# Optimization experiments

Hardware: AMD Instinct MI355X
Metric: run time of the kernel (lower is better)

The kernel has to match this reference:

```python
import jax, jax.numpy as jnp
import numpy as np

N_NODES = 100000
N_EDGES = 3200000
IN_DIM = 128
H1, F1 = 8, 8          # layer1: 8 heads x 8 feats -> concat 64
N_CLASSES = 40         # layer2: 1 head -> classes
NEG_SLOPE = 0.2        # GAT LeakyReLU slope


def setup_inputs() -> dict:
    key = jax.random.key(0)
    ks = jax.random.split(key, 8)
    x = jax.random.normal(ks[0], (N_NODES, IN_DIM), dtype=jnp.float32)
    adj = jax.random.randint(ks[1], (2, N_EDGES), 0, N_NODES, dtype=jnp.int64)
    s1 = 1.0 / np.sqrt(IN_DIM)
    s2 = 1.0 / np.sqrt(H1 * F1)
    W1 = jax.random.normal(ks[2], (IN_DIM, H1 * F1), dtype=jnp.float32) * s1
    a1_src = jax.random.normal(ks[3], (H1, F1), dtype=jnp.float32) * s2
    a1_dst = jax.random.normal(ks[4], (H1, F1), dtype=jnp.float32) * s2
    W2 = jax.random.normal(ks[5], (H1 * F1, N_CLASSES), dtype=jnp.float32) * s2
    a2_src = jax.random.normal(ks[6], (1, N_CLASSES), dtype=jnp.float32) * s2
    a2_dst = jax.random.normal(ks[7], (1, N_CLASSES), dtype=jnp.float32) * s2
    return {"input_matrix": x, "adjacency_coo_matrix": adj,
            "W1": W1, "a1_src": a1_src, "a1_dst": a1_dst,
            "W2": W2, "a2_src": a2_src, "a2_dst": a2_dst}


def gat_layer(x, src, dst, W, a_s, a_d, heads, fdim):
    n = x.shape[0]
    h = (x @ W).reshape(n, heads, fdim)                 # [N,H,F]
    e_src = jnp.sum(h * a_s, axis=-1)                   # [N,H]
    e_dst = jnp.sum(h * a_d, axis=-1)                   # [N,H]
    e = jax.nn.leaky_relu(e_src[src] + e_dst[dst], NEG_SLOPE)  # [E,H]
    m = jax.ops.segment_max(e, dst, num_segments=n)     # per-dst softmax max
    p = jnp.exp(e - m[dst])
    s = jax.ops.segment_sum(p, dst, num_segments=n)
    alpha = p / s[dst]                                  # [E,H]
    out = jax.ops.segment_sum(alpha[:, :, None] * h[src], dst, num_segments=n)
    return out                                          # [N,H,F]


def reference(input_matrix, adjacency_coo_matrix, W1, a1_src, a1_dst, W2, a2_src, a2_dst):
    n = input_matrix.shape[0]
    loops = jnp.arange(n, dtype=adjacency_coo_matrix.dtype)
    src = jnp.concatenate([adjacency_coo_matrix[0], loops])
    dst = jnp.concatenate([adjacency_coo_matrix[1], loops])
    x = gat_layer(input_matrix, src, dst, W1, a1_src, a1_dst, H1, F1)
    x = jax.nn.elu(x.reshape(n, H1 * F1))               # concat heads + ELU
    x = gat_layer(x, src, dst, W2, a2_src, a2_dst, 1, N_CLASSES)
    return jax.nn.log_softmax(x.reshape(n, N_CLASSES), axis=1)
```

## Files before the change

kernel.cpp:

```cpp
#include <hip/hip_runtime.h>
#include <hip/hip_fp16.h>
#include <math.h>

#define NN 100000
#define EE 3200000
#define ET (EE + NN)
#define BKW 128
#define NBK ((NN + BKW - 1) / BKW)
#define BCAP 5120
#define EPB 4096
#define NB_P1 ((EE + EPB - 1) / EPB)
#define NB_G 391

typedef float v2f __attribute__((ext_vector_type(2)));
typedef float v4f __attribute__((ext_vector_type(4)));
typedef _Float16 v8h __attribute__((ext_vector_type(8)));

__device__ __forceinline__ float lrelu(float v) { return fmaxf(v, 0.2f * v); }

__device__ __forceinline__ unsigned char to_fp8(float v) {
  return (unsigned char)(__builtin_amdgcn_cvt_pk_fp8_f32(v, v, 0, false) & 0xff);
}


__global__ __launch_bounds__(256) void k_p1(const int* __restrict__ srcs,
                                            const int* __restrict__ dsts,
                                            int* __restrict__ bcount,
                                            int* __restrict__ bbuf) {
  __shared__ int lcnt[NBK];
  __shared__ int lbase[NBK];
  int tid = threadIdx.x;
  for (int i = tid; i < NBK; i += 256) lcnt[i] = 0;
  __syncthreads();
  int e0 = blockIdx.x * EPB;
  int rank[16], bkt[16], pk[16];
#pragma unroll
  for (int i = 0; i < 16; ++i) {
    int e = e0 + tid + i * 256;
    bkt[i] = -1;
    if (e < EE) {
      int d = dsts[e];
      int s = srcs[e];
      int b = d >> 7;
      rank[i] = atomicAdd(&lcnt[b], 1);
      bkt[i] = b;
      pk[i] = (s << 7) | (d & 127);
    }
  }
  __syncthreads();
  for (int i = tid; i < NBK; i += 256) {
    int c = lcnt[i];
    lbase[i] = c ? atomicAdd(&bcount[i], c) : 0;
  }
  __syncthreads();
#pragma unroll
  for (int i = 0; i < 16; ++i) {
    if (bkt[i] >= 0) {
      bbuf[(size_t)bkt[i] * BCAP + lbase[bkt[i]] + rank[i]] = pk[i];
    }
  }
}

__global__ void k_bscan(const int* __restrict__ bcount, int* __restrict__ bbase) {
  __shared__ int s[1024];
  int t = threadIdx.x;
  int v = 0;
  if (t < NBK) v = bcount[t] + min(BKW, NN - (t << 7));
  s[t] = v;
  __syncthreads();
  for (int off = 1; off < 1024; off <<= 1) {
    int u = (t >= off) ? s[t - off] : 0;
    __syncthreads();
    s[t] += u;
    __syncthreads();
  }
  if (t < NBK) bbase[t] = s[t] - v;
}

__global__ __launch_bounds__(256) void k_p2(const int* __restrict__ bcount,
                                            const int* __restrict__ bbase,
                                            const int* __restrict__ bbuf,
                                            int* __restrict__ offsets,
                                            int* __restrict__ edge_src) {
  __shared__ int cnt[BKW];
  __shared__ int s1[BKW];
  __shared__ int cur[BKW];
  int b = blockIdx.x, tid = threadIdx.x;
  int d0 = b << 7;
  int width = min(BKW, NN - d0);
  int n = bcount[b];
  int base = bbase[b];
  const int* buf = bbuf + (size_t)b * BCAP;
  if (tid < BKW) cnt[tid] = (tid < width) ? 1 : 0;
  __syncthreads();
  for (int i = tid; i < n; i += 256) atomicAdd(&cnt[buf[i] & 127], 1);
  __syncthreads();
  if (tid < BKW) s1[tid] = cnt[tid];
  __syncthreads();
  for (int off = 1; off < BKW; off <<= 1) {
    int u = (tid < BKW && tid >= off) ? s1[tid - off] : 0;
    __syncthreads();
    if (tid < BKW) s1[tid] += u;
    __syncthreads();
  }
  if (tid < width) {
    int excl = s1[tid] - cnt[tid];
    offsets[d0 + tid] = base + excl;
    edge_src[base + excl] = d0 + tid;
    cur[tid] = excl + 1;
  }
  if (b == 0 && tid == 0) offsets[NN] = ET;
  __syncthreads();
  for (int i = tid; i < n; i += 256) {
    int p = buf[i];
    int pos = atomicAdd(&cur[p & 127], 1);
    edge_src[base + pos] = p >> 7;
  }
}


__global__ __launch_bounds__(256) void k_gemm1(
    const float* __restrict__ x, const float* __restrict__ W1,
    const float* __restrict__ a1d,
    unsigned char* __restrict__ P1, float* __restrict__ ed1) {
  __shared__ _Float16 Wb[16 * 64 * 8];
  int tid = threadIdx.x;
  for (int idx = tid; idx < 16 * 64; idx += 256) {
    int f = idx >> 6, l = idx & 63;
    int nt = f >> 2, kk = f & 3;
    int ql = l >> 4, cl = l & 15;
    int col = nt * 16 + cl;
    int k0 = kk * 32 + ql * 8;
    v8h tmp;
#pragma unroll
    for (int j = 0; j < 8; ++j) tmp[j] = (_Float16)W1[(k0 + j) * 64 + col];
    *reinterpret_cast<v8h*>(&Wb[idx * 8]) = tmp;
  }
  __syncthreads();
  int wv = tid >> 6, lane = tid & 63;
  int q = lane >> 4, c = lane & 15;
  v8h bf[16];
#pragma unroll
  for (int f = 0; f < 16; ++f)
    bf[f] = *reinterpret_cast<const v8h*>(&Wb[(f * 64 + lane) * 8]);
  float a1d_l[4];
#pragma unroll
  for (int nt = 0; nt < 4; ++nt) a1d_l[nt] = a1d[nt * 16 + c];
  for (int t = 0; t < 4; ++t) {
    int n0 = blockIdx.x * 256 + wv * 64 + t * 16;
    int row = n0 + c;
    row = (row < NN) ? row : (NN - 1);
    v4f acc[4] = {{0.f,0.f,0.f,0.f},{0.f,0.f,0.f,0.f},{0.f,0.f,0.f,0.f},{0.f,0.f,0.f,0.f}};
#pragma unroll
    for (int kk = 0; kk < 4; ++kk) {
      const float* xp = x + (size_t)row * 128 + kk * 32 + q * 8;
      float4 x0 = *reinterpret_cast<const float4*>(xp);
      float4 x1 = *reinterpret_cast<const float4*>(xp + 4);
      v8h af;
      af[0] = (_Float16)x0.x; af[1] = (_Float16)x0.y;
      af[2] = (_Float16)x0.z; af[3] = (_Float16)x0.w;
      af[4] = (_Float16)x1.x; af[5] = (_Float16)x1.y;
      af[6] = (_Float16)x1.z; af[7] = (_Float16)x1.w;
#pragma unroll
      for (int nt = 0; nt < 4; ++nt)
        acc[nt] = __builtin_amdgcn_mfma_f32_16x16x32_f16(af, bf[nt * 4 + kk], acc[nt], 0, 0, 0);
    }
#pragma unroll
    for (int nt = 0; nt < 4; ++nt) {
#pragma unroll
      for (int r = 0; r < 4; ++r) {
        float val = acc[nt][r];
        float vd = val * a1d_l[nt];
        vd += __shfl_xor(vd, 1); vd += __shfl_xor(vd, 2); vd += __shfl_xor(vd, 4);
        int node = n0 + q * 4 + r;
        if (node < NN) {
          P1[((size_t)node << 6) + nt * 16 + c] = to_fp8(val);
          if ((c & 7) == 0) ed1[node * 8 + 2 * nt + (c >> 3)] = vd;
        }
      }
    }
  }
}


__global__ __launch_bounds__(256) void k_agg1(
    const int* __restrict__ offsets, const int* __restrict__ edge_src,
    const unsigned char* __restrict__ P1, const float* __restrict__ a1s,
    const float* __restrict__ ed1, __half* __restrict__ x2) {
  int wv = threadIdx.x >> 6, lane = threadIdx.x & 63;
  int g = lane >> 3, p = lane & 7;
  int dst = blockIdx.x * 32 + wv * 8 + g;
  float edv = ed1[dst * 8 + p];
  float4 as0 = *reinterpret_cast<const float4*>(a1s + p * 8);
  float4 as1 = *reinterpret_cast<const float4*>(a1s + p * 8 + 4);
  int beg = offsets[dst], end = offsets[dst + 1];
  int deg = end - beg;
  int md = deg;
#pragma unroll
  for (int o = 8; o < 64; o <<= 1) md = max(md, __shfl_xor(md, o, 64));
  float l = 0.f;
  float a[8] = {0.f, 0.f, 0.f, 0.f, 0.f, 0.f, 0.f, 0.f};
  for (int t = 0; t < md; t += 8) {
    int src[8]; uint2 raw[8];
#pragma unroll
    for (int i = 0; i < 8; ++i) {
      int idx = t + i;
      int ci = beg + ((idx < deg) ? idx : (deg - 1));
      src[i] = edge_src[ci];
    }
#pragma unroll
    for (int i = 0; i < 8; ++i)
      raw[i] = *reinterpret_cast<const uint2*>(P1 + ((size_t)src[i] << 6) + (p << 3));
#pragma unroll
    for (int i = 0; i < 8; ++i) {
      v2f f01 = __builtin_amdgcn_cvt_pk_f32_fp8(raw[i].x, false);
      v2f f23 = __builtin_amdgcn_cvt_pk_f32_fp8(raw[i].x, true);
      v2f f45 = __builtin_amdgcn_cvt_pk_f32_fp8(raw[i].y, false);
      v2f f67 = __builtin_amdgcn_cvt_pk_f32_fp8(raw[i].y, true);
      float es = f01.x * as0.x + f01.y * as0.y + f23.x * as0.z + f23.y * as0.w
               + f45.x * as1.x + f45.y * as1.y + f67.x * as1.z + f67.y * as1.w;
      float e = lrelu(es + edv);
      float pr = (t + i < deg) ? __expf(e) : 0.f;
      l += pr;
      a[0] += pr * f01.x; a[1] += pr * f01.y;
      a[2] += pr * f23.x; a[3] += pr * f23.y;
      a[4] += pr * f45.x; a[5] += pr * f45.y;
      a[6] += pr * f67.x; a[7] += pr * f67.y;
    }
  }
  float rl = 1.f / l;
  union { __half h[8]; uint4 u; } pk;
#pragma unroll
  for (int i = 0; i < 8; ++i) {
    float v = a[i] * rl;
    v = (v > 0.f) ? v : (__expf(v) - 1.f);
    pk.h[i] = __float2half(v);
  }
  *reinterpret_cast<uint4*>(x2 + ((size_t)dst << 6) + (p << 3)) = pk.u;
}


__global__ __launch_bounds__(256) void k_gemm2(
    const __half* __restrict__ x2, const float* __restrict__ W2,
    const float* __restrict__ a2s, const float* __restrict__ a2d,
    unsigned char* __restrict__ P2, float* __restrict__ ed2) {
  __shared__ _Float16 Wb[6 * 64 * 8];
  int tid = threadIdx.x;
  for (int idx = tid; idx < 6 * 64; idx += 256) {
    int f = idx >> 6, l = idx & 63;
    int nt = f >> 1, kk = f & 1;
    int ql = l >> 4, cl = l & 15;
    int col = nt * 16 + cl;
    int k0 = kk * 32 + ql * 8;
    v8h tmp;
#pragma unroll
    for (int j = 0; j < 8; ++j)
      tmp[j] = (col < 40) ? (_Float16)W2[(k0 + j) * 40 + col] : (_Float16)0.f;
    *reinterpret_cast<v8h*>(&Wb[idx * 8]) = tmp;
  }
  __syncthreads();
  int wv = tid >> 6, lane = tid & 63;
  int q = lane >> 4, c = lane & 15;
  v8h bf[6];
#pragma unroll
  for (int f = 0; f < 6; ++f)
    bf[f] = *reinterpret_cast<const v8h*>(&Wb[(f * 64 + lane) * 8]);
  float a2s_l[3], a2d_l[3];
#pragma unroll
  for (int nt = 0; nt < 3; ++nt) {
    int n = nt * 16 + c;
    a2s_l[nt] = (n < 40) ? a2s[n] : 0.f;
    a2d_l[nt] = (n < 40) ? a2d[n] : 0.f;
  }
  for (int t = 0; t < 4; ++t) {
    int n0 = blockIdx.x * 256 + wv * 64 + t * 16;
    int row = n0 + c;
    row = (row < NN) ? row : (NN - 1);
    v4f acc[3] = {{0.f,0.f,0.f,0.f},{0.f,0.f,0.f,0.f},{0.f,0.f,0.f,0.f}};
#pragma unroll
    for (int kk = 0; kk < 2; ++kk) {
      v8h af = *reinterpret_cast<const v8h*>(x2 + (size_t)row * 64 + kk * 32 + q * 8);
#pragma unroll
      for (int nt = 0; nt < 3; ++nt)
        acc[nt] = __builtin_amdgcn_mfma_f32_16x16x32_f16(af, bf[nt * 2 + kk], acc[nt], 0, 0, 0);
    }
#pragma unroll
    for (int r = 0; r < 4; ++r) {
      float v0 = acc[0][r], v1 = acc[1][r], v2 = acc[2][r];
      float s = v0 * a2s_l[0] + v1 * a2s_l[1] + v2 * a2s_l[2];
      float d = v0 * a2d_l[0] + v1 * a2d_l[1] + v2 * a2d_l[2];
      s += __shfl_xor(s, 1); s += __shfl_xor(s, 2); s += __shfl_xor(s, 4); s += __shfl_xor(s, 8);
      d += __shfl_xor(d, 1); d += __shfl_xor(d, 2); d += __shfl_xor(d, 4); d += __shfl_xor(d, 8);
      int node = n0 + q * 4 + r;
      if (node < NN) {
        unsigned char* rec = P2 + ((size_t)node << 6);
        if (c < 8) rec[32 + c] = to_fp8(v2);
        rec[c]      = to_fp8(v0);
        rec[16 + c] = to_fp8(v1);
        if (c == 0) {
          *reinterpret_cast<__half*>(rec + 40) = __float2half(s);
          ed2[node] = d;
        }
      }
    }
  }
}


__global__ __launch_bounds__(256) void k_agg2(
    const int* __restrict__ offsets, const int* __restrict__ edge_src,
    const unsigned char* __restrict__ P2, const float* __restrict__ ed2,
    float* __restrict__ out) {
  int wv = threadIdx.x >> 6, lane = threadIdx.x & 63;
  int g = lane >> 4, p = lane & 15;
  bool act = p < 10;
  int cp = act ? p : 0;
  int dst = blockIdx.x * 16 + wv * 4 + g;
  float edv = ed2[dst];
  int beg = offsets[dst], end = offsets[dst + 1];
  int deg = end - beg;
  int md = deg;
#pragma unroll
  for (int o = 16; o < 64; o <<= 1) md = max(md, __shfl_xor(md, o, 64));
  float l = 0.f;
  float a[4] = {0.f, 0.f, 0.f, 0.f};
  for (int t = 0; t < md; t += 8) {
    int src[8]; unsigned raw[8]; float es[8]; float pr[8];
#pragma unroll
    for (int i = 0; i < 8; ++i) {
      int ix = t + i;
      int ci = beg + ((ix < deg) ? ix : (deg - 1));
      src[i] = edge_src[ci];
    }
#pragma unroll
    for (int i = 0; i < 8; ++i) {
      const unsigned char* rec = P2 + ((size_t)src[i] << 6);
      es[i] = __half2float(*reinterpret_cast<const __half*>(rec + 40));
      raw[i] = *reinterpret_cast<const unsigned*>(rec + (cp << 2));
    }
#pragma unroll
    for (int i = 0; i < 8; ++i) {
      float e = lrelu(es[i] + edv);
      pr[i] = (t + i < deg) ? __expf(e) : 0.f;
    }
#pragma unroll
    for (int i = 0; i < 8; ++i) {
      v2f f01 = __builtin_amdgcn_cvt_pk_f32_fp8(raw[i], false);
      v2f f23 = __builtin_amdgcn_cvt_pk_f32_fp8(raw[i], true);
      l += pr[i];
      a[0] += pr[i] * f01.x; a[1] += pr[i] * f01.y;
      a[2] += pr[i] * f23.x; a[3] += pr[i] * f23.y;
    }
  }
  float rl = 1.f / l;
  float v0 = a[0] * rl, v1 = a[1] * rl, v2 = a[2] * rl, v3 = a[3] * rl;
  float red = act ? fmaxf(fmaxf(v0, v1), fmaxf(v2, v3)) : -INFINITY;
#pragma unroll
  for (int o = 1; o < 16; o <<= 1) red = fmaxf(red, __shfl_xor(red, o, 64));
  float se = act ? (__expf(v0 - red) + __expf(v1 - red) + __expf(v2 - red) + __expf(v3 - red)) : 0.f;
#pragma unroll
  for (int o = 1; o < 16; o <<= 1) se += __shfl_xor(se, o, 64);
  float ls = red + __logf(se);
  if (act) {
    float4 o4 = make_float4(v0 - ls, v1 - ls, v2 - ls, v3 - ls);
    *reinterpret_cast<float4*>(out + (size_t)dst * 40 + (p << 2)) = o4;
  }
}


extern "C" void kernel_launch(void* const* d_in, const int* in_sizes, int n_in,
                              void* d_out, int out_size, void* d_ws, size_t ws_size,
                              hipStream_t stream) {
  const float* x   = (const float*)d_in[0];
  const int*   adj = (const int*)d_in[1];
  const float* W1  = (const float*)d_in[2];
  const float* a1s = (const float*)d_in[3];
  const float* a1d = (const float*)d_in[4];
  const float* W2  = (const float*)d_in[5];
  const float* a2s = (const float*)d_in[6];
  const float* a2d = (const float*)d_in[7];
  float* out = (float*)d_out;

  const int* srcs = adj;
  const int* dsts = adj + EE;

  char* w = (char*)d_ws;
  size_t off = 0;
  auto alloc = [&](size_t bytes) -> void* {
    void* p = w + off;
    off = (off + bytes + 255) & ~(size_t)255;
    return p;
  };
  int* offsets      = (int*)alloc((size_t)(NN + 1) * 4);
  int* edge_src     = (int*)alloc((size_t)ET * 4);
  int* bcount       = (int*)alloc((size_t)NBK * 4);
  int* bbase        = (int*)alloc((size_t)NBK * 4);
  unsigned char* P1 = (unsigned char*)alloc((size_t)NN * 64);
  float* ed1        = (float*)alloc((size_t)NN * 8 * 4);
  __half* x2        = (__half*)alloc((size_t)NN * 64 * 2);
  int* bbuf         = (int*)alloc((size_t)NBK * BCAP * 4);
  unsigned char* P2 = P1;
  float* ed2 = ed1;

  hipMemsetAsync(bcount, 0, (size_t)NBK * 4, stream);
  k_p1<<<NB_P1, 256, 0, stream>>>(srcs, dsts, bcount, bbuf);
  k_bscan<<<1, 1024, 0, stream>>>(bcount, bbase);
  k_p2<<<NBK, 256, 0, stream>>>(bcount, bbase, bbuf, offsets, edge_src);

  k_gemm1<<<NB_G, 256, 0, stream>>>(x, W1, a1d, P1, ed1);
  k_agg1<<<NN / 32, 256, 0, stream>>>(offsets, edge_src, P1, a1s, ed1, x2);
  k_gemm2<<<NB_G, 256, 0, stream>>>(x2, W2, a2s, a2d, P2, ed2);
  k_agg2<<<NN / 16, 256, 0, stream>>>(offsets, edge_src, P2, ed2, out);
}
```

Baseline: 311.8 us.

## Split bucket-scatter into count and scatter passes; share edge exp across lanes in agg2

Result: slower. 332.6 us (+6.7%).

```diff
diff --git a/kernel.cpp b/kernel.cpp
--- a/kernel.cpp
+++ b/kernel.cpp
@@ -8,7 +8,7 @@
 #define BKW 128
 #define NBK ((NN + BKW - 1) / BKW)
 #define BCAP 5120
-#define EPB 4096
+#define EPB 8192
 #define NB_P1 ((EE + EPB - 1) / EPB)
 #define NB_G 391
 
@@ -33,31 +33,22 @@
   for (int i = tid; i < NBK; i += 256) lcnt[i] = 0;
   __syncthreads();
   int e0 = blockIdx.x * EPB;
-  int rank[16], bkt[16], pk[16];
-#pragma unroll
-  for (int i = 0; i < 16; ++i) {
-    int e = e0 + tid + i * 256;
-    bkt[i] = -1;
-    if (e < EE) {
-      int d = dsts[e];
-      int s = srcs[e];
-      int b = d >> 7;
-      rank[i] = atomicAdd(&lcnt[b], 1);
-      bkt[i] = b;
-      pk[i] = (s << 7) | (d & 127);
-    }
-  }
+  int e1 = (e0 + EPB < EE) ? (e0 + EPB) : EE;
+  for (int e = e0 + tid; e < e1; e += 256)
+    atomicAdd(&lcnt[dsts[e] >> 7], 1);
   __syncthreads();
   for (int i = tid; i < NBK; i += 256) {
     int c = lcnt[i];
     lbase[i] = c ? atomicAdd(&bcount[i], c) : 0;
   }
   __syncthreads();
-#pragma unroll
-  for (int i = 0; i < 16; ++i) {
-    if (bkt[i] >= 0) {
-      bbuf[(size_t)bkt[i] * BCAP + lbase[bkt[i]] + rank[i]] = pk[i];
-    }
+  for (int i = tid; i < NBK; i += 256) lcnt[i] = 0;
+  __syncthreads();
+  for (int e = e0 + tid; e < e1; e += 256) {
+    int d = dsts[e], s = srcs[e];
+    int b = d >> 7;
+    int r = atomicAdd(&lcnt[b], 1);
+    bbuf[(size_t)b * BCAP + lbase[b] + r] = (s << 7) | (d & 127);
   }
 }
 
@@ -322,34 +313,33 @@
   int md = deg;
 #pragma unroll
   for (int o = 16; o < 64; o <<= 1) md = max(md, __shfl_xor(md, o, 64));
+  int gbase = lane & 48;
+  int me = p & 7;
   float l = 0.f;
   float a[4] = {0.f, 0.f, 0.f, 0.f};
   for (int t = 0; t < md; t += 8) {
-    int src[8]; unsigned raw[8]; float es[8]; float pr[8];
+    int src[8]; unsigned raw[8];
 #pragma unroll
     for (int i = 0; i < 8; ++i) {
       int ix = t + i;
       int ci = beg + ((ix < deg) ? ix : (deg - 1));
       src[i] = edge_src[ci];
     }
+    float myes = __half2float(*reinterpret_cast<const __half*>(
+        P2 + ((size_t)src[me] << 6) + 40));
+    float mye = lrelu(myes + edv);
+    float mypr = (t + me < deg) ? __expf(mye) : 0.f;
+#pragma unroll
+    for (int i = 0; i < 8; ++i)
+      raw[i] = *reinterpret_cast<const unsigned*>(P2 + ((size_t)src[i] << 6) + (cp << 2));
 #pragma unroll
     for (int i = 0; i < 8; ++i) {
-      const unsigned char* rec = P2 + ((size_t)src[i] << 6);
-      es[i] = __half2float(*reinterpret_cast<const __half*>(rec + 40));
-      raw[i] = *reinterpret_cast<const unsigned*>(rec + (cp << 2));
-    }
-#pragma unroll
-    for (int i = 0; i < 8; ++i) {
-      float e = lrelu(es[i] + edv);
-      pr[i] = (t + i < deg) ? __expf(e) : 0.f;
-    }
-#pragma unroll
-    for (int i = 0; i < 8; ++i) {
+      float pr = __shfl(mypr, gbase | i, 64);
       v2f f01 = __builtin_amdgcn_cvt_pk_f32_fp8(raw[i], false);
       v2f f23 = __builtin_amdgcn_cvt_pk_f32_fp8(raw[i], true);
-      l += pr[i];
-      a[0] += pr[i] * f01.x; a[1] += pr[i] * f01.y;
-      a[2] += pr[i] * f23.x; a[3] += pr[i] * f23.y;
+      l += pr;
+      a[0] += pr * f01.x; a[1] += pr * f01.y;
+      a[2] += pr * f23.x; a[3] += pr * f23.y;
     }
   }
   float rl = 1.f / l;
```
